# Optimization experiments

Hardware: AMD Instinct MI355X
Metric: run time of the kernel (lower is better)

The kernel has to match this reference:

```python
import jax, jax.numpy as jnp
import numpy as np

NEG = -1e9          # finite stand-in for -inf (avoids NaN grads, exp underflows to 0)
EPS = float(np.exp(-10.0))


def _pair_tables(L):
    # row-major pair order (i outer), as in nn_utils.batch_feature_selection
    idx = np.zeros((L, L), dtype=np.int32)
    ii, jj = [], []
    c = 0
    for i in range(L - 1):
        for j in range(i + 1, L):
            idx[i, j] = c
            ii.append(i); jj.append(j)
            c += 1
    # rev order (j outer), as in rev_inds_table
    ridx = np.zeros((L, L), dtype=np.int32)
    ri, rj = [], []
    c = 0
    for j in range(1, L):
        for i in range(j):
            ridx[i, j] = c
            ri.append(i); rj.append(j)
            c += 1
    return idx, np.array(ii), np.array(jj), ridx, np.array(ri), np.array(rj)


def _forward(enc, sentence, W1t, b1t, W2t, b2t, W1w, b1w, W2w, b2w):
    L, B, H = enc.shape
    n = L - 1  # sent_length
    idx_tab, ii, jj, rev_tab, ri, rj = _pair_tables(L)

    feats = jnp.concatenate([enc[ii], enc[jj]], axis=-1)        # [P, B, 2H]
    rev_feats = jnp.concatenate([enc[ri], enc[rj]], axis=-1)    # [P, B, 2H]

    def trans_prob(f):  # BinaryClassifier + Sigmoid
        h = jax.nn.relu(f @ W1t + b1t)
        return jax.nn.sigmoid((h @ W2t + b2t)[..., 0])          # [P, B]

    re_p = trans_prob(feats)
    sh_log = jnp.log1p(-re_p + EPS)                              # shift log-probs
    re_rev_log = jnp.log(trans_prob(rev_feats) + EPS)            # reduce log-probs

    def word_logits(f):  # Classifier (pre log-softmax)
        h = jax.nn.relu(f @ W1w + b1w)
        return h @ W2w + b2w

    logits = word_logits(feats)                                  # [P, B, V]
    lse = jax.nn.logsumexp(logits, axis=-1)                      # [P, B]

    # init cell table[0,0,1]: word log-prob of sentence[1] under features (0,0)
    f00 = jnp.concatenate([enc[0], enc[0]], axis=-1)             # [B, 2H]
    l00 = word_logits(f00)
    g00 = jnp.take_along_axis(l00, sentence[1][:, None], axis=1)[:, 0] \
          - jax.nn.logsumexp(l00, axis=-1)

    table = jnp.full((L, L, L, B), NEG, dtype=enc.dtype)
    table = table.at[0, 0, 1].set(g00)

    # base cells: table[i, j, j+1] = log(1-re) + log p(word_{j+1})
    bi, bj = [], []
    for i in range(n - 1):
        for j in range(i + 1, n):
            bi.append(i); bj.append(j)
    bi = np.array(bi); bj = np.array(bj)
    pidx = idx_tab[bi, bj]
    words = sentence[bj + 1]                                     # [Nb, B]
    g = jnp.take_along_axis(logits[pidx], words[:, :, None], axis=2)[:, :, 0] - lse[pidx]
    table = table.at[bi, bj, bj + 1].set(sh_log[pidx] + g)

    # inside recursion over span width (vectorized over i, l, k, batch)
    for gap in range(2, n + 1):
        iv = np.arange(n + 1 - gap)
        jv = iv + gap
        d = np.arange(1, gap)
        kmat = iv[:, None] + d[None, :]                          # [I, gap-1]
        right = table[iv[:, None], kmat, jv[:, None]] \
                + re_rev_log[rev_tab[kmat, jv[:, None]]]         # [I, gap-1, B]
        scores = table[:, iv[:, None], kmat] + right[None]       # [L, I, gap-1, B]
        table = table.at[:, iv, jv].set(jax.nn.logsumexp(scores, axis=2))

    return table[0, 0, n]                                        # [B]


def setup_inputs() -> dict:
    key = jax.random.key(0)
    ks = jax.random.split(key, 8)
    L, B, H, V = 64, 8, 512, 8192
    s = 0.02
    return {
        "enc": jax.random.normal(ks[0], (L, B, H), dtype=jnp.float32),
        "sentence": jax.random.randint(ks[1], (L, B), 0, V),
        "W1t": jax.random.normal(ks[2], (2 * H, H), dtype=jnp.float32) * s,
        "b1t": jnp.zeros((H,), dtype=jnp.float32),
        "W2t": jax.random.normal(ks[3], (H, 1), dtype=jnp.float32) * s,
        "b2t": jnp.zeros((1,), dtype=jnp.float32),
        "W1w": jax.random.normal(ks[4], (2 * H, H), dtype=jnp.float32) * s,
        "b1w": jnp.zeros((H,), dtype=jnp.float32),
        "W2w": jax.random.normal(ks[5], (H, V), dtype=jnp.float32) * s,
        "b2w": jnp.zeros((V,), dtype=jnp.float32),
    }


def reference(enc, sentence, W1t, b1t, W2t, b2t, W1w, b1w, W2w, b2w):
    return _forward(enc, sentence, W1t, b1t, W2t, b2t, W1w, b1w, W2w, b2w)
```

## Files before the change

kernel.cpp:

```cpp
#include <hip/hip_runtime.h>
#include <math.h>

#define LL 64
#define BB 8
#define HH 512
#define H2 1024
#define VV 8192
#define NSENT 63
#define NPAIR 2016
#define NPITEM 2017
#define MROWS 16136
#define MPAD 16256
#define NEGV (-1e9f)
#define EPSV 4.5399929762484854e-05f

typedef unsigned int uint;
typedef unsigned short ushort;
typedef unsigned char uchar;
using f32x4  = __attribute__((ext_vector_type(4))) float;

__device__ inline size_t staged8(int row, int k) {
    return ((size_t)(row >> 4) << 13) + ((size_t)(k >> 5) << 9)
         + (((k >> 3) & 3) << 7) + ((row & 15) << 3) + (k & 7);
}
__device__ inline void gl_lds16(const void* g, void* l) {
    __builtin_amdgcn_global_load_lds(
        (const __attribute__((address_space(1))) unsigned int*)g,
        (__attribute__((address_space(3))) unsigned int*)l, 16, 0, 0);
}
__device__ inline void lse_step(float& m, float& s, float x) {
    float M = fmaxf(m, x);
    s = s * __expf(m - M) + __expf(x - M);
    m = M;
}
__device__ inline void lse_comb(float& m, float& s, float mo, float so) {
    float M = fmaxf(m, mo);
    s = s * __expf(m - M) + so * __expf(mo - M);
    m = M;
}
__device__ inline void tri_decode(int li, int& i, int& l) {
    i = (int)((sqrtf(8.0f * (float)li + 1.0f) - 1.0f) * 0.5f);
    if ((i + 1) * (i + 2) / 2 <= li) i++;
    else if (i * (i + 1) / 2 > li) i--;
    l = li - i * (i + 1) / 2;
}

__global__ __launch_bounds__(256) void ulw2wt_kernel(
    const float* __restrict__ enc, const float* __restrict__ W1t,
    const float* __restrict__ W1w, const float* __restrict__ W2w,
    const int* __restrict__ sentence,
    float* __restrict__ UL, uchar* __restrict__ w2w8,
    int* __restrict__ pair_i, int* __restrict__ pair_j, int* __restrict__ words)
{
    __shared__ float smem[64 * 65];
    if (blockIdx.x >= 1280) {
        const int p = (blockIdx.x - 1280) * 256 + threadIdx.x;
        if (p >= NPITEM) return;
        int i = 0, j = 0;
        if (p != NPAIR) {
            int base = 0;
            while (i < 62 && p >= base + (NSENT - i)) { base += NSENT - i; i++; }
            j = i + 1 + (p - base);
        }
        pair_i[p] = i; pair_j[p] = j;
        for (int b = 0; b < BB; b++) {
            int w;
            if (p == NPAIR)      w = sentence[1 * BB + b];
            else if (j <= 62)    w = sentence[(j + 1) * BB + b];
            else                 w = -1;
            words[p * BB + b] = w;
        }
        return;
    }
    if (blockIdx.x < 1024) {
        const int kt = blockIdx.x >> 7;
        const int nt = blockIdx.x & 127;
        const int k0 = kt * 64, n0 = nt * 64;
        for (int it = 0; it < 16; it++) {
            int idx = it * 256 + threadIdx.x;
            int kr = idx >> 6, nc = idx & 63;
            smem[kr * 65 + nc] = W2w[(size_t)(k0 + kr) * VV + n0 + nc];
        }
        __syncthreads();
        for (int it = 0; it < 8; it++) {
            int idx = it * 256 + threadIdx.x;
            int nr = idx >> 5, kc = (idx & 31) * 2;
            int pk = __builtin_amdgcn_cvt_pk_fp8_f32(
                16.f * smem[kc * 65 + nr], 16.f * smem[(kc + 1) * 65 + nr], 0, false);
            *(ushort*)&w2w8[staged8(n0 + nr, k0 + kc)] = (ushort)pk;
        }
        return;
    }
    const int bid = blockIdx.x - 1024;
    const int mat = bid >> 6;
    const int l = bid & 63;
    float* f = smem;
    for (int t = threadIdx.x; t < BB * HH; t += 256)
        f[t] = enc[(size_t)l * BB * HH + t];
    __syncthreads();

    const float* W = (mat == 0) ? W1t : (mat == 1) ? (W1t + HH * HH)
                   : (mat == 2) ? W1w : (W1w + HH * HH);
    const int u0 = threadIdx.x;
    float acc0[BB], acc1[BB];
#pragma unroll
    for (int b = 0; b < BB; b++) { acc0[b] = 0.f; acc1[b] = 0.f; }
    for (int k = 0; k < HH; k += 4) {
        float4 fk[BB];
#pragma unroll
        for (int b = 0; b < BB; b++) fk[b] = *(const float4*)&f[b * HH + k];
#pragma unroll
        for (int kk = 0; kk < 4; kk++) {
            float w0 = W[(size_t)(k + kk) * HH + u0];
            float w1 = W[(size_t)(k + kk) * HH + u0 + 256];
#pragma unroll
            for (int b = 0; b < BB; b++) {
                float fb = ((const float*)&fk[b])[kk];
                acc0[b] = fmaf(fb, w0, acc0[b]);
                acc1[b] = fmaf(fb, w1, acc1[b]);
            }
        }
    }
    float* outp = UL + (size_t)mat * 512 * 512 + (size_t)(l * BB) * HH;
#pragma unroll
    for (int b = 0; b < BB; b++) {
        outp[b * HH + u0]       = acc0[b];
        outp[b * HH + u0 + 256] = acc1[b];
    }
}

__global__ __launch_bounds__(256) void pairs_kernel(
    const float* __restrict__ UL, const float* __restrict__ b1t,
    const float* __restrict__ W2t, const float* __restrict__ b2t,
    const float* __restrict__ b1w, const int* __restrict__ pair_i,
    const int* __restrict__ pair_j, const int* __restrict__ words,
    const uchar* __restrict__ w2w8, const float* __restrict__ b2w,
    float* __restrict__ sh_log, float* __restrict__ red_log,
    float* __restrict__ red_logT, uchar* __restrict__ h8,
    float* __restrict__ gval)
{
    const int p = blockIdx.x;
    const int i = pair_i[p], j = pair_j[p];
    const float* Ut = UL;
    const float* Lt = UL + 512 * 512;
    const float* Uw = UL + 2 * 512 * 512;
    const float* Lw = UL + 3 * 512 * 512;

    __shared__ float redm[4][BB];
    __shared__ float redg[4][BB];
    const int k0 = threadIdx.x * 2;
    const float2 b1wv = *(const float2*)&b1w[k0];
    const float2 b1tv = *(const float2*)&b1t[k0];
    const float2 w2tv = *(const float2*)&W2t[k0];
    const size_t kpart = ((size_t)(k0 >> 5) << 9) + (((k0 >> 3) & 3) << 7) + (k0 & 7);

    float part[BB], gv[BB];
#pragma unroll
    for (int b = 0; b < BB; b++) {
        const int row = p * BB + b;
        float2 u = *(const float2*)&Uw[(size_t)(i * BB + b) * HH + k0];
        float2 l = *(const float2*)&Lw[(size_t)(j * BB + b) * HH + k0];
        float h0 = u.x + l.x + b1wv.x; h0 = h0 > 0.f ? h0 : 0.f;
        float h1 = u.y + l.y + b1wv.y; h1 = h1 > 0.f ? h1 : 0.f;
        int pk = __builtin_amdgcn_cvt_pk_fp8_f32(h0, h1, 0, false);
        *(ushort*)&h8[((size_t)(row >> 4) << 13) + kpart + ((row & 15) << 3)] = (ushort)pk;
        const int word = words[row];
        if (word >= 0) {
            int wv = *(const ushort*)&w2w8[staged8(word, k0)];
            float w0 = __builtin_amdgcn_cvt_f32_fp8(wv, 0);
            float w1 = __builtin_amdgcn_cvt_f32_fp8(wv, 1);
            gv[b] = (h0 * w0 + h1 * w1) * 0.0625f;
        } else gv[b] = 0.f;
        float2 ut = *(const float2*)&Ut[(size_t)(i * BB + b) * HH + k0];
        float2 lt = *(const float2*)&Lt[(size_t)(j * BB + b) * HH + k0];
        float t0 = ut.x + lt.x + b1tv.x; t0 = t0 > 0.f ? t0 : 0.f;
        float t1 = ut.y + lt.y + b1tv.y; t1 = t1 > 0.f ? t1 : 0.f;
        part[b] = t0 * w2tv.x + t1 * w2tv.y;
    }

#pragma unroll
    for (int off = 32; off > 0; off >>= 1)
#pragma unroll
        for (int b = 0; b < BB; b++) {
            part[b] += __shfl_down(part[b], off, 64);
            gv[b]   += __shfl_down(gv[b], off, 64);
        }
    const int wave = threadIdx.x >> 6, lane = threadIdx.x & 63;
    if (lane == 0)
#pragma unroll
        for (int b = 0; b < BB; b++) { redm[wave][b] = part[b]; redg[wave][b] = gv[b]; }
    __syncthreads();
    if (threadIdx.x < BB) {
        const int b = threadIdx.x;
        const int word = words[p * BB + b];
        if (word >= 0) {
            float g = redg[0][b] + redg[1][b] + redg[2][b] + redg[3][b];
            gval[p * BB + b] = g + b2w[word];
        }
        if (p != NPAIR) {
            float sc = redm[0][b] + redm[1][b] + redm[2][b] + redm[3][b] + b2t[0];
            float pr = 1.f / (1.f + expf(-sc));
            const float rlv = logf(pr + EPSV);
            sh_log[(i * LL + j) * BB + b]   = log1pf(-pr + EPSV);
            red_log[(i * LL + j) * BB + b]  = rlv;
            red_logT[(j * LL + i) * BB + b] = rlv;
        }
    }
}

__global__ __launch_bounds__(256) void gemm_kernel(
    const uchar* __restrict__ h8, const uchar* __restrict__ w2w8,
    const float* __restrict__ b2w, float* __restrict__ part_s)
{
    const int mt = blockIdx.x >> 6;
    const int nt = blockIdx.x & 63;
    __shared__ uchar As[8192];
    __shared__ uchar Bs[8192];

    const int tid = threadIdx.x;
    const int lane = tid & 63, w = tid >> 6;
    const int wm = w >> 1, wn = w & 1;
    const int quad = lane >> 4, l15 = lane & 15;

    f32x4 acc[4][4];
#pragma unroll
    for (int a = 0; a < 4; a++)
#pragma unroll
        for (int b = 0; b < 4; b++) acc[a][b] = (f32x4){0.f, 0.f, 0.f, 0.f};

    for (int kc = 0; kc < 8; kc++) {
        __syncthreads();
#pragma unroll
        for (int s = 0; s < 4; s++) {
            const int slab = w * 4 + s;
            const int rt = slab & 7;
            if (slab < 8) {
                const uchar* g = h8 + ((size_t)(mt * 8 + rt) << 13)
                               + ((size_t)kc << 10) + lane * 16;
                gl_lds16(g, &As[rt * 1024]);
            } else {
                const uchar* g = w2w8 + ((size_t)(nt * 8 + rt) << 13)
                               + ((size_t)kc << 10) + lane * 16;
                gl_lds16(g, &Bs[rt * 1024]);
            }
        }
        __syncthreads();
#pragma unroll
        for (int ks = 0; ks < 2; ks++) {
            long af[4], bfr[4];
#pragma unroll
            for (int fm = 0; fm < 4; fm++)
                af[fm] = *(const long*)&As[(wm * 4 + fm) * 1024 + ks * 512 + quad * 128 + l15 * 8];
#pragma unroll
            for (int fn = 0; fn < 4; fn++)
                bfr[fn] = *(const long*)&Bs[(wn * 4 + fn) * 1024 + ks * 512 + quad * 128 + l15 * 8];
#pragma unroll
            for (int fm = 0; fm < 4; fm++)
#pragma unroll
                for (int fn = 0; fn < 4; fn++)
                    acc[fm][fn] = __builtin_amdgcn_mfma_f32_16x16x32_fp8_fp8(
                        af[fm], bfr[fn], acc[fm][fn], 0, 0, 0);
        }
    }

    float bias[4];
#pragma unroll
    for (int fn = 0; fn < 4; fn++)
        bias[fn] = b2w[nt * 128 + wn * 64 + fn * 16 + l15];
    const int pslot = nt * 2 + wn;
#pragma unroll
    for (int fm = 0; fm < 4; fm++) {
#pragma unroll
        for (int r = 0; r < 4; r++) {
            float s = __expf(acc[fm][0][r] * 0.0625f + bias[0])
                    + __expf(acc[fm][1][r] * 0.0625f + bias[1])
                    + __expf(acc[fm][2][r] * 0.0625f + bias[2])
                    + __expf(acc[fm][3][r] * 0.0625f + bias[3]);
            s += __shfl_xor(s, 1, 64);
            s += __shfl_xor(s, 2, 64);
            s += __shfl_xor(s, 4, 64);
            s += __shfl_xor(s, 8, 64);
            if (l15 == 0) {
                const int grow = mt * 128 + wm * 64 + fm * 16 + quad * 4 + r;
                part_s[(size_t)pslot * MPAD + grow] = s;
            }
        }
    }
}

__global__ __launch_bounds__(256) void combine_kernel(
    const float* __restrict__ part_s, const float* __restrict__ gval,
    const float* __restrict__ sh_log, const int* __restrict__ pair_i,
    const int* __restrict__ pair_j, float* __restrict__ table,
    float* __restrict__ tableB)
{
    const int row = blockIdx.x * 256 + threadIdx.x;
    if (row >= MROWS) return;
    const int p = row >> 3, b = row & 7;
    float S = 0.f;
    for (int nt = 0; nt < 128; nt++)
        S += part_s[(size_t)nt * MPAD + row];
    const float lse = logf(S);
    const float g = gval[row] - lse;
    const int i = pair_i[p], j = pair_j[p];
    if (p == NPAIR) {
        table[(size_t)((0 * LL + 0) * LL + 1) * BB + b]  = g;
        tableB[(size_t)((0 * LL + 1) * LL + 0) * BB + b] = g;
    } else if (j <= 62) {
        const float v = sh_log[(i * LL + j) * BB + b] + g;
        table[(size_t)((i * LL + j) * LL + (j + 1)) * BB + b]  = v;
        tableB[(size_t)((i * LL + (j + 1)) * LL + j) * BB + b] = v;
    }
}

template<int G>
__global__ __launch_bounds__(256) void dp_triple_t(
    const float* __restrict__ red_logT, float* __restrict__ table,
    float* __restrict__ tableB, float* __restrict__ out)
{
    constexpr int NE0 = (64 - G) * (65 - G) / 2;
    constexpr int NE1 = (63 - G) * (64 - G) / 2;
    constexpr int NE2 = (62 - G) * (63 - G) / 2;
    constexpr int E0 = NE0 * 32;
    constexpr int E1 = NE1 * 128;
    const int t = blockIdx.x * 256 + threadIdx.x;

    if (t < E0) {
        const int sub = t & 3;
        const int cell = t >> 2;
        const int b = cell & 7;
        int i, l; tri_decode(cell >> 3, i, l);
        const int j = i + G;
        const float* Tli  = table  + ((size_t)(l * LL + i) * LL) * BB + b;
        const float* TijB = tableB + ((size_t)(i * LL + j) * LL) * BB + b;
        const float* rlT  = red_logT + ((size_t)j * LL) * BB + b;
        float m = -3.4e38f, s = 0.f;
#pragma unroll
        for (int d = 0; d < (G + 2) / 4; d++) {
            const int k = i + 1 + sub + 4 * d;
            const float x = (k < j) ? (Tli[k * 8] + TijB[k * 8] + rlT[k * 8])
                                    : -INFINITY;
            lse_step(m, s, x);
        }
        lse_comb(m, s, __shfl_xor(m, 1, 64), __shfl_xor(s, 1, 64));
        lse_comb(m, s, __shfl_xor(m, 2, 64), __shfl_xor(s, 2, 64));
        if (sub == 0) {
            const float val = m + logf(s);
            table[(((size_t)l * LL + i) * LL + j) * BB + b]  = val;
            tableB[(((size_t)l * LL + j) * LL + i) * BB + b] = val;
        }
        return;
    }

    if (t < E0 + E1) {
        const int o = t - E0;
        const int r = o & 15;
        const int cell = o >> 4;
        const int b = cell & 7;
        int i, l; tri_decode(cell >> 3, i, l);
        const int j = i + G + 1;

        const float* Tli  = table  + ((size_t)(l * LL + i) * LL) * BB + b;
        const float* TijB = tableB + ((size_t)(i * LL + j) * LL) * BB + b;
        const float* rlT  = red_logT + ((size_t)j * LL) * BB + b;

        float m = -3.4e38f, s = 0.f;
        if (r < 4) {
            const float* Tij1B = tableB + ((size_t)(i * LL + (j - 1)) * LL) * BB + b;
            const float* rl1T  = red_logT + ((size_t)(j - 1) * LL) * BB + b;
#pragma unroll
            for (int d = 0; d < (G + 2) / 4; d++) {
                const int k = i + 1 + r + 4 * d;
                const float x = (k < j - 1) ? (Tli[k * 8] + Tij1B[k * 8] + rl1T[k * 8])
                                            : -INFINITY;
                lse_step(m, s, x);
            }
        } else if (r < 8) {
            const float* Ti1k = table  + ((size_t)(i * LL + (i + 1)) * LL) * BB + b;
            const float* TkjB = tableB + ((size_t)((i + 1) * LL + j) * LL) * BB + b;
#pragma unroll
            for (int d = 0; d < (G + 2) / 4; d++) {
                const int k = i + 2 + (r - 4) + 4 * d;
                const float x = (k < j) ? (Ti1k[k * 8] + TkjB[k * 8] + rlT[k * 8])
                                        : -INFINITY;
                lse_step(m, s, x);
            }
        } else {
#pragma unroll
            for (int d = 0; d < (G + 5) / 8; d++) {
                const int k = i + 2 + (r - 8) + 8 * d;
                const float x = (k < j - 1) ? (Tli[k * 8] + TijB[k * 8] + rlT[k * 8])
                                            : -INFINITY;
                lse_step(m, s, x);
            }
        }
        lse_comb(m, s, __shfl_xor(m, 1, 64), __shfl_xor(s, 1, 64));
        lse_comb(m, s, __shfl_xor(m, 2, 64), __shfl_xor(s, 2, 64));
        if (r >= 8)
            lse_comb(m, s, __shfl_xor(m, 4, 64), __shfl_xor(s, 4, 64));
        const int base = (threadIdx.x & 63) & ~15;
        float m1 = __shfl(m, base + 0, 64), s1 = __shfl(s, base + 0, 64);
        float m2 = __shfl(m, base + 4, 64), s2 = __shfl(s, base + 4, 64);
        float M  = __shfl(m, base + 8, 64), S  = __shfl(s, base + 8, 64);
        const float r1 = m1 + logf(s1);
        const float r2 = m2 + logf(s2);
        lse_step(M, S, Tli[(i + 1) * 8] + r2 + rlT[(i + 1) * 8]);
        lse_step(M, S, r1 + TijB[(j - 1) * 8] + rlT[(j - 1) * 8]);
        const float val = M + logf(S);
        if (r == 0) {
            table[(((size_t)l * LL + i) * LL + j) * BB + b]  = val;
            tableB[(((size_t)l * LL + j) * LL + i) * BB + b] = val;
            if (i == 0 && l == 0 && j == NSENT) out[b] = val;
        }
        return;
    }

    const int o2 = t - E0 - E1;
    if (o2 >= NE2 * 256) return;
    const int r = o2 & 31;
    const int cell = o2 >> 5;
    const int b = cell & 7;
    int i, l; tri_decode(cell >> 3, i, l);
    const int j = i + G + 2;

    const float* Tli  = table  + ((size_t)(l * LL + i) * LL) * BB + b;
    const float* Ti1  = table  + ((size_t)(i * LL + (i + 1)) * LL) * BB + b;
    const float* Ti2  = table  + ((size_t)(i * LL + (i + 2)) * LL) * BB + b;
    const float* Ti12 = table  + ((size_t)((i + 1) * LL + (i + 2)) * LL) * BB + b;
    const float* TBiG  = tableB + ((size_t)(i * LL + (i + G)) * LL) * BB + b;
    const float* TB1G1 = tableB + ((size_t)((i + 1) * LL + (i + G + 1)) * LL) * BB + b;
    const float* TB2j  = tableB + ((size_t)((i + 2) * LL + j) * LL) * BB + b;
    const float* TBiG1 = tableB + ((size_t)(i * LL + (i + G + 1)) * LL) * BB + b;
    const float* TB1j  = tableB + ((size_t)((i + 1) * LL + j) * LL) * BB + b;
    const float* TBij  = tableB + ((size_t)(i * LL + j) * LL) * BB + b;
    const float* Rj  = red_logT + ((size_t)j * LL) * BB + b;
    const float* RG  = red_logT + ((size_t)(i + G) * LL) * BB + b;
    const float* RG1 = red_logT + ((size_t)(i + G + 1) * LL) * BB + b;

    const int loop = r >> 2, s4 = r & 3;
    const float *A, *Bp, *R;
    int ks, ke;
    switch (loop) {
        case 0: A = Tli;  Bp = TBiG;  R = RG;  ks = i + 1; ke = i + G;     break;
        case 1: A = Ti1;  Bp = TB1G1; R = RG1; ks = i + 2; ke = i + G + 1; break;
        case 2: A = Ti2;  Bp = TB2j;  R = Rj;  ks = i + 3; ke = i + G + 2; break;
        case 3: A = Ti12; Bp = TB2j;  R = Rj;  ks = i + 3; ke = i + G + 2; break;
        case 4: A = Tli;  Bp = TBiG1; R = RG1; ks = i + 2; ke = i + G;     break;
        case 5: A = Ti1;  Bp = TB1j;  R = Rj;  ks = i + 3; ke = i + G + 1; break;
        case 6: A = Tli;  Bp = TBij;  R = Rj;  ks = i + 3; ke = i + G;     break;
        default: A = Tli; Bp = TBij;  R = Rj;  ks = 0;     ke = 0;         break;
    }
    float m = -3.4e38f, s = 0.f;
#pragma unroll
    for (int d = 0; d < (G + 2) / 4; d++) {
        const int k = ks + s4 + 4 * d;
        const float x = (k < ke) ? (A[k * 8] + Bp[k * 8] + R[k * 8]) : -INFINITY;
        lse_step(m, s, x);
    }
    lse_comb(m, s, __shfl_xor(m, 1, 64), __shfl_xor(s, 1, 64));
    lse_comb(m, s, __shfl_xor(m, 2, 64), __shfl_xor(s, 2, 64));
    const int wb = (threadIdx.x & 63) & ~31;
    float mv[7], sv[7];
#pragma unroll
    for (int q = 0; q < 7; q++) {
        mv[q] = __shfl(m, wb + 4 * q, 64);
        sv[q] = __shfl(s, wb + 4 * q, 64);
    }
    const float P1v = mv[0] + logf(sv[0]);
    const float P3v = mv[1] + logf(sv[1]);
    const float P4v = mv[2] + logf(sv[2]);
    const float P6v = mv[3] + logf(sv[3]);
    float m2 = mv[4], s2 = sv[4];
    lse_step(m2, s2, Tli[(i + 1) * 8] + P3v + RG1[(i + 1) * 8]);
    lse_step(m2, s2, P1v + table[(((size_t)i * LL + (i + G)) * LL + (i + G + 1)) * BB + b]
                     + RG1[(i + G) * 8]);
    const float P2v = m2 + logf(s2);
    float m5 = mv[5], s5 = sv[5];
    lse_step(m5, s5, Ti1[(i + 2) * 8] + P6v + Rj[(i + 2) * 8]);
    lse_step(m5, s5, P3v + table[(((size_t)(i + 1) * LL + (i + G + 1)) * LL + j) * BB + b]
                     + Rj[(i + G + 1) * 8]);
    const float P5v = m5 + logf(s5);
    float M = mv[6], S = sv[6];
    lse_step(M, S, Tli[(i + 1) * 8] + P5v + Rj[(i + 1) * 8]);
    lse_step(M, S, P2v + table[(((size_t)i * LL + (i + G + 1)) * LL + j) * BB + b]
                   + Rj[(i + G + 1) * 8]);
    if (G > 2) {
        lse_step(M, S, Tli[(i + 2) * 8] + P4v + Rj[(i + 2) * 8]);
        lse_step(M, S, P1v + table[(((size_t)i * LL + (i + G)) * LL + j) * BB + b]
                       + Rj[(i + G) * 8]);
    } else {
        lse_step(M, S, P1v + P4v + Rj[(i + 2) * 8]);
    }
    const float val = M + logf(S);
    if (r == 0) {
        table[(((size_t)l * LL + i) * LL + j) * BB + b]  = val;
        tableB[(((size_t)l * LL + j) * LL + i) * BB + b] = val;
    }
}

static void launch_dp(int G, const float* red_logT, float* table, float* tableB,
                      float* out, hipStream_t stream) {
    const int NE0 = (64 - G) * (65 - G) / 2;
    const int NE1 = (63 - G) * (64 - G) / 2;
    const int NE2 = (62 - G) * (63 - G) / 2;
    const int total = NE0 * 32 + NE1 * 128 + NE2 * 256;
    const int blocks = (total + 255) / 256;
#define DPC(GG) case GG: dp_triple_t<GG><<<blocks, 256, 0, stream>>>(red_logT, table, tableB, out); break;
    switch (G) {
        DPC(2)  DPC(5)  DPC(8)  DPC(11) DPC(14) DPC(17) DPC(20)
        DPC(23) DPC(26) DPC(29) DPC(32) DPC(35) DPC(38) DPC(41)
        DPC(44) DPC(47) DPC(50) DPC(53) DPC(56) DPC(59) DPC(62)
    }
#undef DPC
}

extern "C" void kernel_launch(void* const* d_in, const int* in_sizes, int n_in,
                              void* d_out, int out_size, void* d_ws, size_t ws_size,
                              hipStream_t stream) {
    const float* enc      = (const float*)d_in[0];
    const int*   sentence = (const int*)  d_in[1];
    const float* W1t      = (const float*)d_in[2];
    const float* b1t      = (const float*)d_in[3];
    const float* W2t      = (const float*)d_in[4];
    const float* b2t      = (const float*)d_in[5];
    const float* W1w      = (const float*)d_in[6];
    const float* b1w      = (const float*)d_in[7];
    const float* W2w      = (const float*)d_in[8];
    const float* b2w      = (const float*)d_in[9];
    float* out = (float*)d_out;

    float* base = (float*)d_ws;
    float* table    = base;                base += (size_t)LL * LL * LL * BB;
    float* tableB   = base;                base += (size_t)LL * LL * LL * BB;
    float* sh_log   = base;                base += LL * LL * BB;
    float* red_log  = base;                base += LL * LL * BB;
    float* red_logT = base;                base += LL * LL * BB;
    float* UL       = base;                base += 4 * 512 * 512;
    float* part_s   = base;                base += (size_t)128 * MPAD;
    float* gval     = base;                base += MPAD;
    int*   words    = (int*)base;          base += MPAD;
    int*   pair_i   = (int*)base;          base += 2048;
    int*   pair_j   = (int*)base;          base += 2048;
    uchar* h8       = (uchar*)base;        base += (size_t)MPAD * HH / 4;
    uchar* w2w8     = (uchar*)base;        base += (size_t)VV * HH / 4;

    ulw2wt_kernel<<<1288, 256, 0, stream>>>(enc, W1t, W1w, W2w, sentence,
                                            UL, w2w8, pair_i, pair_j, words);
    pairs_kernel<<<NPITEM, 256, 0, stream>>>(UL, b1t, W2t, b2t, b1w,
                                             pair_i, pair_j, words, w2w8, b2w,
                                             sh_log, red_log, red_logT, h8, gval);
    gemm_kernel<<<127 * 64, 256, 0, stream>>>(h8, w2w8, b2w, part_s);
    combine_kernel<<<64, 256, 0, stream>>>(part_s, gval, sh_log, pair_i, pair_j,
                                           table, tableB);
    for (int G = 2; G <= 62; G += 3)
        launch_dp(G, red_logT, table, tableB, out, stream);
}
```

Measured before the change: 498.7 us.

## Use MI355 scaled 16x16x128 FP8 MFMA with direct register loads in GEMM

Switches the vocab GEMM from the 16x16x32 FP8 MFMA to the gfx950 scaled 16x16x128 f8f6f4 MFMA with unit scales. The staged FP8 layout for h8 and w2w8 changes to 32-byte K chunks per row, so each lane loads its 32-byte operands straight from global memory. This drops the LDS staging and both __syncthreads, and a register double buffer prefetches the next K chunk. The cost is higher register pressure and no LDS sharing of operands across waves, so each wave re-reads its A and B tiles from global/L2.

```diff
diff --git a/kernel.cpp b/kernel.cpp
--- a/kernel.cpp
+++ b/kernel.cpp
@@ -17,16 +17,12 @@
 typedef unsigned int uint;
 typedef unsigned short ushort;
 typedef unsigned char uchar;
-using f32x4  = __attribute__((ext_vector_type(4))) float;
+using f32x4 = __attribute__((ext_vector_type(4))) float;
+using i32x8 = __attribute__((ext_vector_type(8))) int;
 
 __device__ inline size_t staged8(int row, int k) {
-    return ((size_t)(row >> 4) << 13) + ((size_t)(k >> 5) << 9)
-         + (((k >> 3) & 3) << 7) + ((row & 15) << 3) + (k & 7);
-}
-__device__ inline void gl_lds16(const void* g, void* l) {
-    __builtin_amdgcn_global_load_lds(
-        (const __attribute__((address_space(1))) unsigned int*)g,
-        (__attribute__((address_space(3))) unsigned int*)l, 16, 0, 0);
+    return ((size_t)(row >> 4) << 13) + ((size_t)(k >> 7) << 11)
+         + ((size_t)((((k >> 5) & 3) * 16 + (row & 15))) << 5) + (k & 31);
 }
 __device__ inline void lse_step(float& m, float& s, float x) {
     float M = fmaxf(m, x);
@@ -152,7 +148,8 @@
     const float2 b1wv = *(const float2*)&b1w[k0];
     const float2 b1tv = *(const float2*)&b1t[k0];
     const float2 w2tv = *(const float2*)&W2t[k0];
-    const size_t kpart = ((size_t)(k0 >> 5) << 9) + (((k0 >> 3) & 3) << 7) + (k0 & 7);
+    const size_t kpart = ((size_t)(k0 >> 7) << 11) + ((size_t)((k0 >> 5) & 3) << 9)
+                       + (k0 & 31);
 
     float part[BB], gv[BB];
 #pragma unroll
@@ -163,7 +160,8 @@
         float h0 = u.x + l.x + b1wv.x; h0 = h0 > 0.f ? h0 : 0.f;
         float h1 = u.y + l.y + b1wv.y; h1 = h1 > 0.f ? h1 : 0.f;
         int pk = __builtin_amdgcn_cvt_pk_fp8_f32(h0, h1, 0, false);
-        *(ushort*)&h8[((size_t)(row >> 4) << 13) + kpart + ((row & 15) << 3)] = (ushort)pk;
+        *(ushort*)&h8[((size_t)(row >> 4) << 13) + kpart + ((size_t)(row & 15) << 5)]
+            = (ushort)pk;
         const int word = words[row];
         if (word >= 0) {
             int wv = *(const ushort*)&w2w8[staged8(word, k0)];
@@ -214,8 +212,6 @@
 {
     const int mt = blockIdx.x >> 6;
     const int nt = blockIdx.x & 63;
-    __shared__ uchar As[8192];
-    __shared__ uchar Bs[8192];
 
     const int tid = threadIdx.x;
     const int lane = tid & 63, w = tid >> 6;
@@ -228,38 +224,33 @@
 #pragma unroll
         for (int b = 0; b < 4; b++) acc[a][b] = (f32x4){0.f, 0.f, 0.f, 0.f};
 
-    for (int kc = 0; kc < 8; kc++) {
-        __syncthreads();
-#pragma unroll
-        for (int s = 0; s < 4; s++) {
-            const int slab = w * 4 + s;
-            const int rt = slab & 7;
-            if (slab < 8) {
-                const uchar* g = h8 + ((size_t)(mt * 8 + rt) << 13)
-                               + ((size_t)kc << 10) + lane * 16;
-                gl_lds16(g, &As[rt * 1024]);
-            } else {
-                const uchar* g = w2w8 + ((size_t)(nt * 8 + rt) << 13)
-                               + ((size_t)kc << 10) + lane * 16;
-                gl_lds16(g, &Bs[rt * 1024]);
+    const uchar* aBase = h8   + (((size_t)(mt * 8 + wm * 4)) << 13) + lane * 32;
+    const uchar* bBase = w2w8 + (((size_t)(nt * 8 + wn * 4)) << 13) + lane * 32;
+
+    i32x8 af[4], bf[4], an[4], bn[4];
+#pragma unroll
+    for (int f = 0; f < 4; f++) {
+        af[f] = *(const i32x8*)(aBase + ((size_t)f << 13));
+        bf[f] = *(const i32x8*)(bBase + ((size_t)f << 13));
+    }
+    for (int kc = 0; kc < 4; kc++) {
+        if (kc < 3) {
+            const size_t co = (size_t)(kc + 1) << 11;
+#pragma unroll
+            for (int f = 0; f < 4; f++) {
+                an[f] = *(const i32x8*)(aBase + ((size_t)f << 13) + co);
+                bn[f] = *(const i32x8*)(bBase + ((size_t)f << 13) + co);
             }
         }
-        __syncthreads();
-#pragma unroll
-        for (int ks = 0; ks < 2; ks++) {
-            long af[4], bfr[4];
-#pragma unroll
-            for (int fm = 0; fm < 4; fm++)
-                af[fm] = *(const long*)&As[(wm * 4 + fm) * 1024 + ks * 512 + quad * 128 + l15 * 8];
+#pragma unroll
+        for (int fm = 0; fm < 4; fm++)
 #pragma unroll
             for (int fn = 0; fn < 4; fn++)
-                bfr[fn] = *(const long*)&Bs[(wn * 4 + fn) * 1024 + ks * 512 + quad * 128 + l15 * 8];
-#pragma unroll
-            for (int fm = 0; fm < 4; fm++)
-#pragma unroll
-                for (int fn = 0; fn < 4; fn++)
-                    acc[fm][fn] = __builtin_amdgcn_mfma_f32_16x16x32_fp8_fp8(
-                        af[fm], bfr[fn], acc[fm][fn], 0, 0, 0);
+                acc[fm][fn] = __builtin_amdgcn_mfma_scale_f32_16x16x128_f8f6f4(
+                    af[fm], bf[fn], acc[fm][fn], 0, 0, 0, 0x7F, 0, 0x7F);
+        if (kc < 3) {
+#pragma unroll
+            for (int f = 0; f < 4; f++) { af[f] = an[f]; bf[f] = bn[f]; }
         }
     }
 
```

Result: slower. 540.3 us (+8.3%).
